# Performance work log

Measured on AMD Instinct MI355X. Metric: run time of the kernel, lower is better.

The kernel has to match this reference:

```python
import jax, jax.numpy as jnp
import numpy as np

CC = 0.25        # commitment_cost
BN_EPS = 1e-5    # BatchNorm1d eps (eval mode, running_mean=0, running_var=1)
EPS_PPL = 1e-10


def _res_block(x, W1, b1, W2, b2, gamma, beta):
    # Linear(D,16) -> ReLU -> Linear(16,D) -> ReLU -> BatchNorm1d(eval), residual add
    h = jax.nn.relu(x @ W1 + b1)
    h = jax.nn.relu(h @ W2 + b2)
    h = h / jnp.sqrt(1.0 + BN_EPS) * gamma + beta
    return x + h


def setup_inputs() -> dict:
    B, IN, L1, D, ED, K = 512, 4096, 2048, 512, 64, 512
    key = jax.random.key(0)
    ks = iter(jax.random.split(key, 48))

    def rn(shape, s=0.02):
        return (jax.random.normal(next(ks), shape) * s).astype(jnp.float32)

    z = lambda *s: jnp.zeros(s, jnp.float32)
    inp = {
        "x": jax.random.normal(next(ks), (B, IN), dtype=jnp.float32),
        # encoder
        "We1": rn((IN, L1)), "be1": z(L1),
        "We2": rn((L1, D)), "be2": z(D),
        "Wre1": rn((D, 16)), "bre1": z(16), "Wre2": rn((16, D)), "bre2": z(D),
        "ge": jnp.ones((D,), jnp.float32), "bebn": z(D),
        # VQ
        "E": jax.random.uniform(next(ks), (K, ED), jnp.float32, -1.0 / K, 1.0 / K),
        "Wt1": rn((1, ED // 2)), "bt1": z(ED // 2),
        "Wt2": rn((ED // 2, ED)), "bt2": z(ED),
        "Wc": rn((ED * D, 10)), "bc": z(10),
        # decoder
        "Wp": rn((ED * D, D)), "bp": z(D),
        "Wrd1": rn((D, 16)), "brd1": z(16), "Wrd2": rn((16, D)), "brd2": z(D),
        "gd": jnp.ones((D,), jnp.float32), "bdbn": z(D),
        "Wd1": rn((D, L1)), "bd1": z(L1),
        "Wd2": rn((L1, IN)), "bd2": z(IN),
    }
    return inp


def reference(x, We1, be1, We2, be2, Wre1, bre1, Wre2, bre2, ge, bebn,
              E, Wt1, bt1, Wt2, bt2, Wc, bc,
              Wp, bp, Wrd1, brd1, Wrd2, brd2, gd, bdbn, Wd1, bd1, Wd2, bd2):
    # ---- Encoder (dropout = identity in eval) ----
    h = jax.nn.relu(x @ We1 + be1)          # [B, enc_lay1]
    zenc = jax.nn.relu(h @ We2 + be2)       # [B, enc_dim]
    zenc = _res_block(zenc, Wre1, bre1, Wre2, bre2, ge, bebn)

    # ---- VectorQuantizer ----
    B, D = zenc.shape
    e = jax.nn.relu(zenc[..., None] @ Wt1 + bt1) @ Wt2 + bt2   # [B, D, ED]
    ED = e.shape[-1]
    K = E.shape[0]
    flat = e.reshape(-1, ED)                                    # [(B*D), ED]
    dist = (jnp.sum(flat * flat, axis=1, keepdims=True)
            + jnp.sum(E * E, axis=1)
            - 2.0 * flat @ E.T)                                 # [(B*D), K]
    idx = jnp.argmin(dist, axis=1)                              # [(B*D)]
    q = E[idx].reshape(B, D, ED)                                # gather == onehot @ E
    counts = jnp.zeros((K,), flat.dtype).at[idx].add(1.0) / idx.shape[0]

    cls = jax.nn.sigmoid(q.reshape(B, D * ED) @ Wc + bc)        # [B, 10]

    e_loss = jnp.mean((jax.lax.stop_gradient(q) - e) ** 2)
    q_loss = jnp.mean((q - jax.lax.stop_gradient(e)) ** 2)
    vq_loss = q_loss + CC * e_loss

    q_st = (e + jax.lax.stop_gradient(q - e)).reshape(B, D * ED)  # straight-through
    p = jax.lax.stop_gradient(counts)
    perplexity = jnp.exp(-jnp.sum(p * jnp.log(p + EPS_PPL)))

    # ---- Decoder ----
    d = jax.nn.relu(q_st @ Wp + bp)
    d = _res_block(d, Wrd1, brd1, Wrd2, brd2, gd, bdbn)
    d = jax.nn.relu(d @ Wd1 + bd1)
    x_recon = jax.nn.relu(d @ Wd2 + bd2)
    return (vq_loss, x_recon, perplexity, q_st, cls, zenc)
```

## Files before the change

kernel.cpp:

```cpp
#include <hip/hip_runtime.h>

typedef unsigned int uint;

enum { ACT_RELU=0, ACT_SIGMOID=1, ACT_RESBN=2 };

template<int ACT>
__global__ __launch_bounds__(256) void gemm_fused(
    const float* __restrict__ A, const float* __restrict__ W,
    const float* __restrict__ bias, float* __restrict__ C,
    float* __restrict__ C2, const float* __restrict__ R,
    const float* __restrict__ gamma, const float* __restrict__ beta,
    int M, int N, int K)
{
    __shared__ float As[16][68];
    __shared__ float Bs[16][68];
    const int tx = threadIdx.x, ty = threadIdx.y;
    const int tid = ty*16 + tx;
    const int row0 = blockIdx.y*64, col0 = blockIdx.x*64;
    float acc[4][4] = {};
    for (int k0 = 0; k0 < K; k0 += 16) {
        #pragma unroll
        for (int t = tid; t < 1024; t += 256) {
            int r = t >> 4, c = t & 15;
            As[c][r] = A[(size_t)(row0+r)*K + k0 + c];
        }
        #pragma unroll
        for (int t = tid; t < 1024; t += 256) {
            int kr = t >> 6, c = t & 63;
            int gc = col0 + c;
            Bs[kr][c] = (gc < N) ? W[(size_t)(k0+kr)*N + gc] : 0.f;
        }
        __syncthreads();
        #pragma unroll
        for (int kk = 0; kk < 16; kk++) {
            float a[4], b[4];
            #pragma unroll
            for (int i = 0; i < 4; i++) a[i] = As[kk][ty*4+i];
            #pragma unroll
            for (int j = 0; j < 4; j++) b[j] = Bs[kk][tx*4+j];
            #pragma unroll
            for (int i = 0; i < 4; i++)
                #pragma unroll
                for (int j = 0; j < 4; j++)
                    acc[i][j] += a[i]*b[j];
        }
        __syncthreads();
    }
    const float INVS = 0.99999500003749968f;
    #pragma unroll
    for (int i = 0; i < 4; i++) {
        int r = row0 + ty*4 + i;
        #pragma unroll
        for (int j = 0; j < 4; j++) {
            int c = col0 + tx*4 + j;
            if (c < N) {
                float v = acc[i][j] + bias[c];
                if (ACT == ACT_RELU) {
                    v = fmaxf(v, 0.f);
                } else if (ACT == ACT_SIGMOID) {
                    v = 1.f/(1.f + expf(-v));
                } else {
                    v = fmaxf(v, 0.f);
                    v = v*(gamma[c]*INVS) + beta[c];
                    v += R[(size_t)r*N + c];
                }
                C[(size_t)r*N + c] = v;
                if (C2) C2[(size_t)r*N + c] = v;
            }
        }
    }
}

__global__ __launch_bounds__(256) void gemm_acc(
    const float* __restrict__ A, const float* __restrict__ W,
    float* __restrict__ C, int M, int N, int K, int kchunk)
{
    __shared__ float As[16][68];
    __shared__ float Bs[16][68];
    const int tx = threadIdx.x, ty = threadIdx.y;
    const int tid = ty*16 + tx;
    const int row0 = blockIdx.y*64, col0 = blockIdx.x*64;
    const int kbeg = blockIdx.z * kchunk, kend = kbeg + kchunk;
    float acc[4][4] = {};
    for (int k0 = kbeg; k0 < kend; k0 += 16) {
        #pragma unroll
        for (int t = tid; t < 1024; t += 256) {
            int r = t >> 4, c = t & 15;
            As[c][r] = A[(size_t)(row0+r)*K + k0 + c];
        }
        #pragma unroll
        for (int t = tid; t < 1024; t += 256) {
            int kr = t >> 6, c = t & 63;
            int gc = col0 + c;
            Bs[kr][c] = (gc < N) ? W[(size_t)(k0+kr)*N + gc] : 0.f;
        }
        __syncthreads();
        #pragma unroll
        for (int kk = 0; kk < 16; kk++) {
            float a[4], b[4];
            #pragma unroll
            for (int i = 0; i < 4; i++) a[i] = As[kk][ty*4+i];
            #pragma unroll
            for (int j = 0; j < 4; j++) b[j] = Bs[kk][tx*4+j];
            #pragma unroll
            for (int i = 0; i < 4; i++)
                #pragma unroll
                for (int j = 0; j < 4; j++)
                    acc[i][j] += a[i]*b[j];
        }
        __syncthreads();
    }
    #pragma unroll
    for (int i = 0; i < 4; i++) {
        int r = row0 + ty*4 + i;
        #pragma unroll
        for (int j = 0; j < 4; j++) {
            int c = col0 + tx*4 + j;
            if (c < N) atomicAdd(&C[(size_t)r*N + c], acc[i][j]);
        }
    }
}

template<int ACT>
__global__ __launch_bounds__(256) void epi_k(
    float* __restrict__ C, const float* __restrict__ bias,
    float* __restrict__ dst, int M, int N)
{
    int i = blockIdx.x*256 + threadIdx.x;
    if (i >= M*N) return;
    int c = i % N;
    float v = C[i] + bias[c];
    if (ACT == ACT_RELU) v = fmaxf(v, 0.f);
    else v = 1.f/(1.f + expf(-v));
    C[i] = v;
    if (dst) dst[i] = v;
}

__global__ __launch_bounds__(256) void zero_k(float* __restrict__ p, int n)
{
    int i = blockIdx.x*256 + threadIdx.x;
    if (i < n) p[i] = 0.f;
}

__global__ __launch_bounds__(256) void esq2_k(
    const float* __restrict__ E, const float* __restrict__ bt2,
    const float* __restrict__ Wt2,
    float* __restrict__ C2, float* __restrict__ Hm2)
{
    int k = blockIdx.x*256 + threadIdx.x;
    if (k >= 512) return;
    const float4* Er = (const float4*)(E + (size_t)k*64);
    const float4* b4 = (const float4*)bt2;
    float esq = 0.f, g0 = 0.f;
    #pragma unroll
    for (int m = 0; m < 16; m++) {
        float4 w = Er[m]; float4 b = b4[m];
        esq += w.x*w.x + w.y*w.y + w.z*w.z + w.w*w.w;
        g0  += b.x*w.x + b.y*w.y + b.z*w.z + b.w*w.w;
    }
    C2[k] = esq - 2.f*g0;
    for (int i = 0; i < 32; i++) {
        const float4* Wr = (const float4*)(Wt2 + i*64);
        float h = 0.f;
        #pragma unroll
        for (int m = 0; m < 16; m++) {
            float4 w = Er[m]; float4 ww = Wr[m];
            h += w.x*ww.x + w.y*ww.y + w.z*ww.z + w.w*ww.w;
        }
        Hm2[(size_t)k*32 + i] = -2.f*h;
    }
}

__global__ __launch_bounds__(256) void vqc_k(
    const float* __restrict__ zencf, const float* __restrict__ Wt1,
    const float* __restrict__ bt1, const float* __restrict__ bt2,
    const float* __restrict__ Wt2, const float* __restrict__ E,
    const float* __restrict__ C2, const float* __restrict__ Hm2,
    float* __restrict__ qout, float* __restrict__ hist,
    float* __restrict__ sspart)
{
    __shared__ float aT[32][256];
    __shared__ int   rowbi[256];
    __shared__ int   hcnt[512];
    __shared__ float red4[4];
    const int tid = threadIdx.x;
    const int gid = blockIdx.x*256 + tid;
    const float z = zencf[gid];

    hcnt[tid] = 0; hcnt[tid + 256] = 0;

    float a[32];
    #pragma unroll
    for (int i = 0; i < 32; i++) {
        a[i] = fmaxf(z*Wt1[i] + bt1[i], 0.f);
        aT[i][tid] = a[i];
    }
    __syncthreads();

    float best = 3.4e38f; int bi = 0;
    for (int k = 0; k < 512; k++) {
        const float* hp = Hm2 + k*32;
        float s = C2[k];
        #pragma unroll
        for (int i = 0; i < 32; i++) s = fmaf(a[i], hp[i], s);
        if (s < best) { best = s; bi = k; }
    }
    atomicAdd(&hcnt[bi], 1);
    rowbi[tid] = bi;

    float ls = 0.f;
    const float4* Eq = (const float4*)(E + (size_t)bi*64);
    const float4* b4 = (const float4*)bt2;
    for (int m = 0; m < 16; m++) {
        float4 w = Eq[m];
        float4 e4 = b4[m];
        #pragma unroll 8
        for (int i = 0; i < 32; i++) {
            float ai = aT[i][tid];
            float4 wr = *(const float4*)(Wt2 + i*64 + 4*m);
            e4.x = fmaf(ai, wr.x, e4.x);
            e4.y = fmaf(ai, wr.y, e4.y);
            e4.z = fmaf(ai, wr.z, e4.z);
            e4.w = fmaf(ai, wr.w, e4.w);
        }
        float d;
        d = w.x - e4.x; ls += d*d;
        d = w.y - e4.y; ls += d*d;
        d = w.z - e4.z; ls += d*d;
        d = w.w - e4.w; ls += d*d;
    }
    #pragma unroll
    for (int off = 32; off > 0; off >>= 1)
        ls += __shfl_down(ls, off, 64);
    if ((tid & 63) == 0) red4[tid >> 6] = ls;

    __syncthreads();

    if (tid == 0)
        sspart[blockIdx.x] = ((red4[0] + red4[1]) + red4[2]) + red4[3];
    hist[(size_t)blockIdx.x*512 + tid]       = (float)hcnt[tid];
    hist[(size_t)blockIdx.x*512 + 256 + tid] = (float)hcnt[tid + 256];

    const int wid  = tid >> 6;
    const int lane = tid & 63;
    float2* qo2w = (float2*)qout + ((size_t)blockIdx.x*8192 + (size_t)wid*2048);
    const int rbase = wid*64;
    #pragma unroll 4
    for (int c = 0; c < 32; c++) {
        const int idx2 = c*64 + lane;
        const int r    = rbase + (idx2 >> 5);
        const int d2   = idx2 & 31;
        const int bir  = rowbi[r];
        float2 w2 = *((const float2*)(E + (size_t)bir*64) + d2);
        qo2w[idx2] = w2;
    }
}

__global__ __launch_bounds__(512) void finalize_k(
    const float* __restrict__ hist, const float* __restrict__ sspart,
    float* __restrict__ out)
{
    __shared__ float red[512];
    int tid = threadIdx.x;
    float c = 0.f;
    for (int b = 0; b < 1024; b++) c += hist[(size_t)b*512 + tid];
    red[tid] = sspart[tid] + sspart[tid + 512];
    __syncthreads();
    for (int s = 256; s > 0; s >>= 1) { if (tid < s) red[tid] += red[tid+s]; __syncthreads(); }
    float ss = red[0];
    __syncthreads();
    float p = c * (1.f/262144.f);
    red[tid] = p * logf(p + 1e-10f);
    __syncthreads();
    for (int s = 256; s > 0; s >>= 1) { if (tid < s) red[tid] += red[tid+s]; __syncthreads(); }
    if (tid == 0) {
        out[0]       = 1.25f * ss * (1.f/16777216.f);
        out[2097153] = expf(-red[0]);
    }
}

extern "C" void kernel_launch(void* const* d_in, const int* in_sizes, int n_in,
                              void* d_out, int out_size, void* d_ws, size_t ws_size,
                              hipStream_t stream)
{
    const float* x    = (const float*)d_in[0];
    const float* We1  = (const float*)d_in[1];  const float* be1  = (const float*)d_in[2];
    const float* We2  = (const float*)d_in[3];  const float* be2  = (const float*)d_in[4];
    const float* Wre1 = (const float*)d_in[5];  const float* bre1 = (const float*)d_in[6];
    const float* Wre2 = (const float*)d_in[7];  const float* bre2 = (const float*)d_in[8];
    const float* ge   = (const float*)d_in[9];  const float* bebn = (const float*)d_in[10];
    const float* E    = (const float*)d_in[11];
    const float* Wt1  = (const float*)d_in[12]; const float* bt1  = (const float*)d_in[13];
    const float* Wt2  = (const float*)d_in[14]; const float* bt2  = (const float*)d_in[15];
    const float* Wc   = (const float*)d_in[16]; const float* bc   = (const float*)d_in[17];
    const float* Wp   = (const float*)d_in[18]; const float* bp   = (const float*)d_in[19];
    const float* Wrd1 = (const float*)d_in[20]; const float* brd1 = (const float*)d_in[21];
    const float* Wrd2 = (const float*)d_in[22]; const float* brd2 = (const float*)d_in[23];
    const float* gd   = (const float*)d_in[24]; const float* bdbn = (const float*)d_in[25];
    const float* Wd1  = (const float*)d_in[26]; const float* bd1  = (const float*)d_in[27];
    const float* Wd2  = (const float*)d_in[28]; const float* bd2  = (const float*)d_in[29];

    float* out    = (float*)d_out;
    float* o_xr   = out + 1;
    float* o_q    = out + 2097154;
    float* o_cls  = out + 18874370;
    float* o_zenc = out + 18879490;

    float* ws    = (float*)d_ws;
    float* sumsq = ws + 0;
    float* cnts  = ws + 16;
    float* t1    = ws + 528;
    float* t2    = ws + 8720;
    float* clsf  = ws + 16912;
    float* z0    = ws + 22032;
    float* dp0   = ws + 284176;
    float* zencf = ws + 546320;
    float* dd    = ws + 808464;
    float* hbuf  = ws + 1070608;
    float* d2    = ws + 1070608;
    float* c2t   = ws + 1070608;
    float* hm2t  = ws + 1071120;
    float* hist  = ws + 1087504;
    float* sspart= ws + 1611792;

    dim3 blk(16, 16);

    zero_k<<<dim3(2135), dim3(256), 0, stream>>>(ws, 546320);

    gemm_fused<ACT_RELU><<<dim3(32, 8), blk, 0, stream>>>(
        x, We1, be1, hbuf, nullptr, nullptr, nullptr, nullptr, 512, 2048, 4096);
    gemm_acc<<<dim3(8, 8, 4), blk, 0, stream>>>(hbuf, We2, z0, 512, 512, 2048, 512);
    epi_k<ACT_RELU><<<dim3(1024), dim3(256), 0, stream>>>(z0, be2, nullptr, 512, 512);
    gemm_acc<<<dim3(1, 8, 32), blk, 0, stream>>>(z0, Wre1, t1, 512, 16, 512, 16);
    epi_k<ACT_RELU><<<dim3(32), dim3(256), 0, stream>>>(t1, bre1, nullptr, 512, 16);
    gemm_fused<ACT_RESBN><<<dim3(8, 8), blk, 0, stream>>>(
        t1, Wre2, bre2, zencf, o_zenc, z0, ge, bebn, 512, 512, 16);

    esq2_k<<<dim3(2), dim3(256), 0, stream>>>(E, bt2, Wt2, c2t, hm2t);
    vqc_k<<<dim3(1024), dim3(256), 0, stream>>>(zencf, Wt1, bt1, bt2, Wt2, E,
                                                c2t, hm2t, o_q, hist, sspart);
    finalize_k<<<dim3(1), dim3(512), 0, stream>>>(hist, sspart, out);

    gemm_acc<<<dim3(1, 8, 32), blk, 0, stream>>>(o_q, Wc, clsf, 512, 10, 32768, 1024);
    epi_k<ACT_SIGMOID><<<dim3(20), dim3(256), 0, stream>>>(clsf, bc, o_cls, 512, 10);

    gemm_acc<<<dim3(8, 8, 8), blk, 0, stream>>>(o_q, Wp, dp0, 512, 512, 32768, 4096);
    epi_k<ACT_RELU><<<dim3(1024), dim3(256), 0, stream>>>(dp0, bp, nullptr, 512, 512);
    gemm_acc<<<dim3(1, 8, 32), blk, 0, stream>>>(dp0, Wrd1, t2, 512, 16, 512, 16);
    epi_k<ACT_RELU><<<dim3(32), dim3(256), 0, stream>>>(t2, brd1, nullptr, 512, 16);
    gemm_fused<ACT_RESBN><<<dim3(8, 8), blk, 0, stream>>>(
        t2, Wrd2, brd2, dd, nullptr, dp0, gd, bdbn, 512, 512, 16);
    gemm_fused<ACT_RELU><<<dim3(32, 8), blk, 0, stream>>>(
        dd, Wd1, bd1, d2, nullptr, nullptr, nullptr, nullptr, 512, 2048, 512);
    gemm_fused<ACT_RELU><<<dim3(64, 8), blk, 0, stream>>>(
        d2, Wd2, bd2, o_xr, nullptr, nullptr, nullptr, nullptr, 512, 4096, 2048);
}
```

Before: 2.838 ms.

## Use 128x128 register-tiled split-K GEMM for the large encoder/decoder matmuls

Adds a gemm_big kernel with 128x128 block tiles, 8x8 per-thread register tiles, float4 loads and register prefetch of the next K slice. It is used with split-K and atomic accumulation for the large encoder, projection and decoder GEMMs. Bias and ReLU move to separate epilogue passes, and the output buffers are zeroed first. This is meant to raise arithmetic intensity and occupancy across CUs over the 64x64 tiles. In exchange it adds atomics, extra zeroing and epilogue memory passes.

```diff
diff --git a/kernel.cpp b/kernel.cpp
--- a/kernel.cpp
+++ b/kernel.cpp
@@ -121,6 +121,84 @@
     }
 }
 
+__device__ inline float4 ld4_a8(const float* p) {
+    float2 lo = *(const float2*)p;
+    float2 hi = *(const float2*)(p + 2);
+    return make_float4(lo.x, lo.y, hi.x, hi.y);
+}
+
+template<bool A16>
+__global__ __launch_bounds__(256)
+__attribute__((amdgpu_waves_per_eu(2, 4)))
+void gemm_big(
+    const float* __restrict__ A, const float* __restrict__ W,
+    float* __restrict__ C, int M, int N, int K, int kchunk)
+{
+    __shared__ float As[16][132];
+    __shared__ float Bs[16][132];
+    const int tid = threadIdx.x;
+    const int tx = tid & 15, ty = tid >> 4;
+    const int row0 = blockIdx.y*128, col0 = blockIdx.x*128;
+    const size_t kbeg = (size_t)blockIdx.z * kchunk;
+
+    const int ar0 = tid >> 2;
+    const int ac0 = (tid & 3) * 4;
+    const int ar1 = ar0 + 64;
+    const int bk0 = tid >> 5;
+    const int bc0 = (tid & 31) * 4;
+    const int bk1 = bk0 + 8;
+
+    const float* Ap0 = A + (size_t)(row0 + ar0)*K + kbeg + ac0;
+    const float* Ap1 = A + (size_t)(row0 + ar1)*K + kbeg + ac0;
+    const float* Bp0 = W + (kbeg + bk0)*(size_t)N + col0 + bc0;
+    const float* Bp1 = W + (kbeg + bk1)*(size_t)N + col0 + bc0;
+
+    float4 pa0 = A16 ? *(const float4*)Ap0 : ld4_a8(Ap0);
+    float4 pa1 = A16 ? *(const float4*)Ap1 : ld4_a8(Ap1);
+    float4 pb0 = *(const float4*)Bp0;
+    float4 pb1 = *(const float4*)Bp1;
+
+    float acc[8][8] = {};
+
+    for (int k0 = 0; k0 < kchunk; k0 += 16) {
+        As[ac0+0][ar0] = pa0.x; As[ac0+1][ar0] = pa0.y;
+        As[ac0+2][ar0] = pa0.z; As[ac0+3][ar0] = pa0.w;
+        As[ac0+0][ar1] = pa1.x; As[ac0+1][ar1] = pa1.y;
+        As[ac0+2][ar1] = pa1.z; As[ac0+3][ar1] = pa1.w;
+        *(float4*)&Bs[bk0][bc0] = pb0;
+        *(float4*)&Bs[bk1][bc0] = pb1;
+        __syncthreads();
+        if (k0 + 16 < kchunk) {
+            pa0 = A16 ? *(const float4*)(Ap0 + k0 + 16) : ld4_a8(Ap0 + k0 + 16);
+            pa1 = A16 ? *(const float4*)(Ap1 + k0 + 16) : ld4_a8(Ap1 + k0 + 16);
+            pb0 = *(const float4*)(Bp0 + (size_t)(k0+16)*N);
+            pb1 = *(const float4*)(Bp1 + (size_t)(k0+16)*N);
+        }
+        #pragma unroll
+        for (int kk = 0; kk < 16; kk++) {
+            float a[8], b[8];
+            *(float4*)&a[0] = *(const float4*)&As[kk][ty*8];
+            *(float4*)&a[4] = *(const float4*)&As[kk][ty*8+4];
+            *(float4*)&b[0] = *(const float4*)&Bs[kk][tx*8];
+            *(float4*)&b[4] = *(const float4*)&Bs[kk][tx*8+4];
+            #pragma unroll
+            for (int i = 0; i < 8; i++)
+                #pragma unroll
+                for (int j = 0; j < 8; j++)
+                    acc[i][j] += a[i]*b[j];
+        }
+        __syncthreads();
+    }
+
+    #pragma unroll
+    for (int i = 0; i < 8; i++) {
+        float* crow = C + (size_t)(row0 + ty*8 + i)*N + col0 + tx*8;
+        #pragma unroll
+        for (int j = 0; j < 8; j++)
+            atomicAdd(crow + j, acc[i][j]);
+    }
+}
+
 template<int ACT>
 __global__ __launch_bounds__(256) void epi_k(
     float* __restrict__ C, const float* __restrict__ bias,
@@ -307,8 +385,6 @@
     float* o_zenc = out + 18879490;
 
     float* ws    = (float*)d_ws;
-    float* sumsq = ws + 0;
-    float* cnts  = ws + 16;
     float* t1    = ws + 528;
     float* t2    = ws + 8720;
     float* clsf  = ws + 16912;
@@ -326,10 +402,14 @@
     dim3 blk(16, 16);
 
     zero_k<<<dim3(2135), dim3(256), 0, stream>>>(ws, 546320);
-
-    gemm_fused<ACT_RELU><<<dim3(32, 8), blk, 0, stream>>>(
-        x, We1, be1, hbuf, nullptr, nullptr, nullptr, nullptr, 512, 2048, 4096);
-    gemm_acc<<<dim3(8, 8, 4), blk, 0, stream>>>(hbuf, We2, z0, 512, 512, 2048, 512);
+    zero_k<<<dim3(4096), dim3(256), 0, stream>>>(hbuf, 1048576);
+    zero_k<<<dim3(8192), dim3(256), 0, stream>>>(o_xr, 2097152);
+
+    gemm_big<true><<<dim3(16, 4, 8), dim3(256), 0, stream>>>(
+        x, We1, hbuf, 512, 2048, 4096, 512);
+    epi_k<ACT_RELU><<<dim3(4096), dim3(256), 0, stream>>>(hbuf, be1, nullptr, 512, 2048);
+    gemm_big<true><<<dim3(4, 4, 32), dim3(256), 0, stream>>>(
+        hbuf, We2, z0, 512, 512, 2048, 64);
     epi_k<ACT_RELU><<<dim3(1024), dim3(256), 0, stream>>>(z0, be2, nullptr, 512, 512);
     gemm_acc<<<dim3(1, 8, 32), blk, 0, stream>>>(z0, Wre1, t1, 512, 16, 512, 16);
     epi_k<ACT_RELU><<<dim3(32), dim3(256), 0, stream>>>(t1, bre1, nullptr, 512, 16);
@@ -344,14 +424,18 @@
     gemm_acc<<<dim3(1, 8, 32), blk, 0, stream>>>(o_q, Wc, clsf, 512, 10, 32768, 1024);
     epi_k<ACT_SIGMOID><<<dim3(20), dim3(256), 0, stream>>>(clsf, bc, o_cls, 512, 10);
 
-    gemm_acc<<<dim3(8, 8, 8), blk, 0, stream>>>(o_q, Wp, dp0, 512, 512, 32768, 4096);
+    gemm_big<false><<<dim3(4, 4, 32), dim3(256), 0, stream>>>(
+        o_q, Wp, dp0, 512, 512, 32768, 1024);
     epi_k<ACT_RELU><<<dim3(1024), dim3(256), 0, stream>>>(dp0, bp, nullptr, 512, 512);
     gemm_acc<<<dim3(1, 8, 32), blk, 0, stream>>>(dp0, Wrd1, t2, 512, 16, 512, 16);
     epi_k<ACT_RELU><<<dim3(32), dim3(256), 0, stream>>>(t2, brd1, nullptr, 512, 16);
     gemm_fused<ACT_RESBN><<<dim3(8, 8), blk, 0, stream>>>(
         t2, Wrd2, brd2, dd, nullptr, dp0, gd, bdbn, 512, 512, 16);
-    gemm_fused<ACT_RELU><<<dim3(32, 8), blk, 0, stream>>>(
-        dd, Wd1, bd1, d2, nullptr, nullptr, nullptr, nullptr, 512, 2048, 512);
-    gemm_fused<ACT_RELU><<<dim3(64, 8), blk, 0, stream>>>(
-        d2, Wd2, bd2, o_xr, nullptr, nullptr, nullptr, nullptr, 512, 4096, 2048);
-}
+    zero_k<<<dim3(4096), dim3(256), 0, stream>>>(d2, 1048576);
+    gemm_big<true><<<dim3(16, 4, 8), dim3(256), 0, stream>>>(
+        dd, Wd1, d2, 512, 2048, 512, 64);
+    epi_k<ACT_RELU><<<dim3(4096), dim3(256), 0, stream>>>(d2, bd1, nullptr, 512, 2048);
+    gemm_big<true><<<dim3(32, 4, 4), dim3(256), 0, stream>>>(
+        d2, Wd2, o_xr, 512, 4096, 2048, 512);
+    epi_k<ACT_RELU><<<dim3(8192), dim3(256), 0, stream>>>(o_xr, bd2, nullptr, 512, 4096);
+}
```

Result: faster. 2.387 ms (-15.9%).
